# Kernel tuning notes

Hardware: AMD Instinct MI355X
Metric: run time of the kernel (lower is better)

The kernel has to match this reference:

```python
import jax, jax.numpy as jnp
import numpy as np

B, S, E = 2, 2048, 2048
H, HD = 32, 64          # n_heads, head_dim
KV, REP = 8, 4          # n_kv_head, n_kv_head_rep (H == KV*REP)
NEG = -1e9


def setup_inputs() -> dict:
    key = jax.random.key(0)
    ks = jax.random.split(key, 6)
    x = jax.random.normal(ks[0], (B, S, E), dtype=jnp.float32)
    # Llama RoPE tables: angles[p, i] = p / 10000^(2i/HD)
    inv_freq = 1.0 / (10000.0 ** (jnp.arange(0, HD, 2, dtype=jnp.float32) / HD))
    angles = jnp.arange(S, dtype=jnp.float32)[:, None] * inv_freq[None, :]  # [S, HD/2]
    cos, sin = jnp.cos(angles), jnp.sin(angles)
    # causal additive mask [S, S]
    mask = jnp.where(jnp.tril(jnp.ones((S, S), dtype=bool)), 0.0, NEG).astype(jnp.float32)
    sc = 0.02
    wq = jax.random.normal(ks[1], (E, H * HD), dtype=jnp.float32) * sc
    wk = jax.random.normal(ks[2], (E, KV * HD), dtype=jnp.float32) * sc
    wv = jax.random.normal(ks[3], (E, KV * HD), dtype=jnp.float32) * sc
    wo = jax.random.normal(ks[4], (H * HD, E), dtype=jnp.float32) * sc
    return {"x": x, "cos": cos, "sin": sin, "mask": mask,
            "wq": wq, "wk": wk, "wv": wv, "wo": wo, "start_pos": 0}


def _rope(t, cos, sin):
    # t: [B, S, h, HD]; rotate consecutive pairs (Llama complex convention)
    tp = t.reshape(t.shape[:-1] + (HD // 2, 2))
    t1, t2 = tp[..., 0], tp[..., 1]
    c = cos[None, :, None, :]
    s = sin[None, :, None, :]
    out = jnp.stack([t1 * c - t2 * s, t1 * s + t2 * c], axis=-1)
    return out.reshape(t.shape)


def reference(x, cos, sin, mask, wq, wk, wv, wo, start_pos):
    b, s, _ = x.shape
    q = (x @ wq).reshape(b, s, H, HD)
    k = (x @ wk).reshape(b, s, KV, HD)
    v = (x @ wv).reshape(b, s, KV, HD)
    q = _rope(q, cos, sin)
    k = _rope(k, cos, sin)
    # KV-cache: with start_pos=0 and full-seq prefill, the cache slice
    # [:, :start_pos+s] is exactly the freshly written k/v, so use them directly.
    # Grouped attention without materializing repeated K/V:
    # q -> [b, KV, REP, s, HD]; k,v -> [b, KV, s, HD]
    qg = q.transpose(0, 2, 1, 3).reshape(b, KV, REP, s, HD)
    kg = k.transpose(0, 2, 1, 3)
    vg = v.transpose(0, 2, 1, 3)
    scale = 1.0 / jnp.sqrt(jnp.float32(HD))
    scores = jnp.einsum('bgrqd,bgkd->bgrqk', qg, kg) * scale + mask
    attn = jax.nn.softmax(scores, axis=-1)
    og = jnp.einsum('bgrqk,bgkd->bgrqd', attn, vg)     # [b, KV, REP, s, HD]
    out = og.reshape(b, H, s, HD).transpose(0, 2, 1, 3).reshape(b, s, H * HD)
    return out @ wo
```

## Files before the change

### kernel.cpp

```cpp
#include <hip/hip_runtime.h>
#include <stdint.h>

#define S_LEN 2048
#define NTOK  4096
#define EMB   2048
#define NHEAD 32
#define HDIM  64
#define NKVH  8

typedef __bf16 bf16x8 __attribute__((ext_vector_type(8)));
typedef float  f32x4  __attribute__((ext_vector_type(4)));

#define AS1 __attribute__((address_space(1)))
#define AS3 __attribute__((address_space(3)))

#if __has_builtin(__builtin_amdgcn_exp2f)
#define EXP2(x) __builtin_amdgcn_exp2f(x)
#else
#define EXP2(x) exp2f(x)
#endif

#define QSCALE 0.1803368867f

__device__ __forceinline__ uint16_t f2bf(float f) {
  uint32_t u = __float_as_uint(f);
  u += 0x7fffu + ((u >> 16) & 1u);
  return (uint16_t)(u >> 16);
}
__device__ __forceinline__ float bf2f(uint16_t h) {
  return __uint_as_float(((uint32_t)h) << 16);
}
__device__ __forceinline__ void gld16(const void* g, void* l) {
  __builtin_amdgcn_global_load_lds((const AS1 uint32_t*)g, (AS3 uint32_t*)l, 16, 0, 0);
}
__device__ __forceinline__ f32x4 mfma16(bf16x8 a, bf16x8 b, f32x4 c) {
  return __builtin_amdgcn_mfma_f32_16x16x32_bf16(a, b, c, 0, 0, 0);
}

__global__ void k_cvt(const float* __restrict__ in, uint16_t* __restrict__ out) {
  int i = (blockIdx.x * 256 + threadIdx.x) * 4;
  float4 v = *(const float4*)(in + i);
  ushort4 o;
  o.x = f2bf(v.x); o.y = f2bf(v.y); o.z = f2bf(v.z); o.w = f2bf(v.w);
  *(ushort4*)(out + i) = o;
}

__global__ void k_transpose(const float* __restrict__ in, uint16_t* __restrict__ out,
                            int R, int C) {
  __shared__ float tile[32][33];
  int c0 = blockIdx.x * 32, r0 = blockIdx.y * 32;
  int tx = threadIdx.x & 31, ty = threadIdx.x >> 5;
#pragma unroll
  for (int j = 0; j < 32; j += 8)
    tile[ty + j][tx] = in[(size_t)(r0 + ty + j) * C + c0 + tx];
  __syncthreads();
#pragma unroll
  for (int j = 0; j < 32; j += 8)
    out[(size_t)(c0 + ty + j) * R + r0 + tx] = f2bf(tile[tx][ty + j]);
}

__global__ void k_transpose_v(const uint16_t* __restrict__ in, uint16_t* __restrict__ out) {
  __shared__ uint16_t tile[32][33];
  int s0 = blockIdx.x * 32, hd0 = blockIdx.y * 32, bh = blockIdx.z;
  int b = bh >> 3, kvh = bh & 7;
  int tx = threadIdx.x & 31, ty = threadIdx.x >> 5;
#pragma unroll
  for (int j = 0; j < 32; j += 8)
    tile[ty + j][tx] = in[((size_t)b * S_LEN + s0 + ty + j) * 512 + kvh * 64 + hd0 + tx];
  __syncthreads();
#pragma unroll
  for (int j = 0; j < 32; j += 8)
    out[((size_t)bh * 64 + hd0 + ty + j) * S_LEN + s0 + tx] = tile[tx][ty + j];
}

template <int N_REP, typename OUT_T>
__global__ __launch_bounds__(512, 2) void k_gemm256(
    const uint16_t* __restrict__ A, const uint16_t* __restrict__ BT,
    OUT_T* __restrict__ C, int M, int N, int K) {
  constexpr int ROUNDS = 4 + N_REP;
  __shared__ uint16_t lds[2][16384 + N_REP * 4096];
  const int tid = threadIdx.x, lane = tid & 63, w = tid >> 6;
  const int wm = w >> 2, wn = w & 3;
  const int l16 = lane & 15, lg = lane >> 4;
  const int nbn = N / (N_REP * 64);
  const int nwg = gridDim.x, cpx = nwg >> 3;
  const int swz = ((int)blockIdx.x & 7) * cpx + ((int)blockIdx.x >> 3);
  const int bm = (swz / nbn) * 256, bn = (swz % nbn) * (N_REP * 64);

  f32x4 acc[8][N_REP] = {};

  const int srow = tid >> 3, sslot = tid & 7;
  const int schunk = (sslot ^ (srow & 7)) * 8;
  const uint16_t* Ag = A + (size_t)(bm + srow) * K + schunk;
  const uint16_t* Bg = BT + (size_t)(bn + srow) * K + schunk;

  auto stage = [&](int d, int r, int k0) {
    if (r < 4) gld16(Ag + (size_t)r * 64 * K + k0, &lds[d][r * 4096 + tid * 8]);
    else       gld16(Bg + (size_t)(r - 4) * 64 * K + k0, &lds[d][16384 + (r - 4) * 4096 + tid * 8]);
  };
  auto lda = [&](int d, int mf, int s) -> bf16x8 {
    int row = wm * 128 + mf * 16 + l16;
    int slot = (s * 4 + lg) ^ (row & 7);
    return *(const bf16x8*)(&lds[d][row * 64 + slot * 8]);
  };
  auto ldb = [&](int d, int nf, int s) -> bf16x8 {
    int row = wn * (N_REP * 16) + nf * 16 + l16;
    int slot = (s * 4 + lg) ^ (row & 7);
    return *(const bf16x8*)(&lds[d][16384 + row * 64 + slot * 8]);
  };

  const int NT = K >> 6;
#pragma unroll
  for (int r = 0; r < ROUNDS; ++r) stage(0, r, 0);
#pragma unroll
  for (int r = 0; r < 4; ++r) if (1 < NT) stage(1, r, 64);
  asm volatile("s_waitcnt vmcnt(4)" ::: "memory");
  __builtin_amdgcn_s_barrier();

  for (int kt = 0; kt < NT; ++kt) {
    const int cur = kt & 1;
    const int nk0 = (kt + 1) << 6, nnk0 = (kt + 2) << 6;
    const bool m1 = (kt + 1 < NT), m2 = (kt + 2 < NT);
    bf16x8 a[4][2], b0[N_REP / 2][2], b1[N_REP / 2][2];
#pragma unroll
    for (int mi = 0; mi < 4; ++mi) { a[mi][0] = lda(cur, mi, 0); a[mi][1] = lda(cur, mi, 1); }
#pragma unroll
    for (int ni = 0; ni < N_REP / 2; ++ni) { b0[ni][0] = ldb(cur, ni, 0); b0[ni][1] = ldb(cur, ni, 1); }
    __builtin_amdgcn_s_barrier();
    asm volatile("s_waitcnt lgkmcnt(0)" ::: "memory");
    __builtin_amdgcn_sched_barrier(0);
    __builtin_amdgcn_s_setprio(1);
#pragma unroll
    for (int mi = 0; mi < 4; ++mi)
#pragma unroll
      for (int ni = 0; ni < N_REP / 2; ++ni) {
        acc[mi][ni] = mfma16(a[mi][0], b0[ni][0], acc[mi][ni]);
        acc[mi][ni] = mfma16(a[mi][1], b0[ni][1], acc[mi][ni]);
      }
    __builtin_amdgcn_s_setprio(0);
    __builtin_amdgcn_s_barrier();
#pragma unroll
    for (int ni = 0; ni < N_REP / 2; ++ni) { b1[ni][0] = ldb(cur, N_REP / 2 + ni, 0); b1[ni][1] = ldb(cur, N_REP / 2 + ni, 1); }
    if (m1) {
#pragma unroll
      for (int r = 4; r < 4 + N_REP / 2; ++r) stage(cur ^ 1, r, nk0);
    }
    __builtin_amdgcn_s_barrier();
    asm volatile("s_waitcnt lgkmcnt(0)" ::: "memory");
    __builtin_amdgcn_sched_barrier(0);
    __builtin_amdgcn_s_setprio(1);
#pragma unroll
    for (int mi = 0; mi < 4; ++mi)
#pragma unroll
      for (int ni = 0; ni < N_REP / 2; ++ni) {
        acc[mi][N_REP / 2 + ni] = mfma16(a[mi][0], b1[ni][0], acc[mi][N_REP / 2 + ni]);
        acc[mi][N_REP / 2 + ni] = mfma16(a[mi][1], b1[ni][1], acc[mi][N_REP / 2 + ni]);
      }
    __builtin_amdgcn_s_setprio(0);
    __builtin_amdgcn_s_barrier();
#pragma unroll
    for (int mi = 0; mi < 4; ++mi) { a[mi][0] = lda(cur, 4 + mi, 0); a[mi][1] = lda(cur, 4 + mi, 1); }
    if (m1) {
#pragma unroll
      for (int r = 4 + N_REP / 2; r < ROUNDS; ++r) stage(cur ^ 1, r, nk0);
    }
    __builtin_amdgcn_s_barrier();
    asm volatile("s_waitcnt lgkmcnt(0)" ::: "memory");
    __builtin_amdgcn_sched_barrier(0);
    __builtin_amdgcn_s_setprio(1);
#pragma unroll
    for (int mi = 0; mi < 4; ++mi)
#pragma unroll
      for (int ni = 0; ni < N_REP / 2; ++ni) {
        acc[4 + mi][N_REP / 2 + ni] = mfma16(a[mi][0], b1[ni][0], acc[4 + mi][N_REP / 2 + ni]);
        acc[4 + mi][N_REP / 2 + ni] = mfma16(a[mi][1], b1[ni][1], acc[4 + mi][N_REP / 2 + ni]);
      }
    __builtin_amdgcn_s_setprio(0);
    __builtin_amdgcn_s_barrier();
    if (m2) {
#pragma unroll
      for (int r = 0; r < 4; ++r) stage(cur, r, nnk0);
    }
    __builtin_amdgcn_s_setprio(1);
#pragma unroll
    for (int mi = 0; mi < 4; ++mi)
#pragma unroll
      for (int ni = 0; ni < N_REP / 2; ++ni) {
        acc[4 + mi][ni] = mfma16(a[mi][0], b0[ni][0], acc[4 + mi][ni]);
        acc[4 + mi][ni] = mfma16(a[mi][1], b0[ni][1], acc[4 + mi][ni]);
      }
    __builtin_amdgcn_s_setprio(0);
    if (m2) { asm volatile("s_waitcnt vmcnt(4)" ::: "memory"); }
    else    { asm volatile("s_waitcnt vmcnt(0)" ::: "memory"); }
    __builtin_amdgcn_s_barrier();
  }
#pragma unroll
  for (int mf = 0; mf < 8; ++mf)
#pragma unroll
    for (int nf = 0; nf < N_REP; ++nf)
#pragma unroll
      for (int r = 0; r < 4; ++r) {
        int row = bm + wm * 128 + mf * 16 + lg * 4 + r;
        int col = bn + wn * (N_REP * 16) + nf * 16 + l16;
        float v = acc[mf][nf][r];
        if constexpr (sizeof(OUT_T) == 4) C[(size_t)row * N + col] = v;
        else                              C[(size_t)row * N + col] = f2bf(v);
      }
}

__global__ void k_rope(const uint16_t* __restrict__ qkv, const float* __restrict__ cosT,
                       const float* __restrict__ sinT, uint16_t* __restrict__ qb,
                       uint16_t* __restrict__ kb, uint16_t* __restrict__ vb) {
  int idx = blockIdx.x * 256 + threadIdx.x;
  int row = idx / 1536;
  int col = (idx - row * 1536) * 2;
  int s = row & (S_LEN - 1);
  uint32_t vv = *(const uint32_t*)(qkv + (size_t)row * 3072 + col);
  float t1 = bf2f((uint16_t)vv), t2 = bf2f((uint16_t)(vv >> 16));
  if (col < 2048) {
    int i = (col & 63) >> 1;
    float c = cosT[s * 32 + i] * QSCALE, sn = sinT[s * 32 + i] * QSCALE;
    uint32_t o = (uint32_t)f2bf(t1 * c - t2 * sn) | ((uint32_t)f2bf(t1 * sn + t2 * c) << 16);
    *(uint32_t*)(qb + (size_t)row * 2048 + col) = o;
  } else if (col < 2560) {
    int cc = col - 2048;
    int i = (cc & 63) >> 1;
    float c = cosT[s * 32 + i], sn = sinT[s * 32 + i];
    uint32_t o = (uint32_t)f2bf(t1 * c - t2 * sn) | ((uint32_t)f2bf(t1 * sn + t2 * c) << 16);
    *(uint32_t*)(kb + (size_t)row * 512 + cc) = o;
  } else {
    int cc = col - 2560;
    *(uint32_t*)(vb + (size_t)row * 512 + cc) = vv;
  }
}

template <bool MASKED>
__device__ __forceinline__ void tile_compute(
    const uint16_t* Kc, const uint16_t* Vc, const bf16x8 qf[2][2], bf16x8 onesv,
    int l16, int lg, int kv0, int qb0,
    float m_r[2], f32x4 lacc[2], f32x4 acc[2][4]) {
  f32x4 st[2][4] = {};
  __builtin_amdgcn_s_setprio(1);
#pragma unroll
  for (int c = 0; c < 4; ++c) {
    int row = c * 16 + l16, sw = row & 7;
    bf16x8 ka  = *(const bf16x8*)(Kc + row * 64 + ((lg ^ sw) * 8));
    bf16x8 kb2 = *(const bf16x8*)(Kc + row * 64 + (((4 | lg) ^ sw) * 8));
#pragma unroll
    for (int qc = 0; qc < 2; ++qc) {
      st[qc][c] = mfma16(ka,  qf[qc][0], st[qc][c]);
      st[qc][c] = mfma16(kb2, qf[qc][1], st[qc][c]);
    }
  }
  __builtin_amdgcn_s_setprio(0);
  bf16x8 pu[2][2];
#pragma unroll
  for (int qc = 0; qc < 2; ++qc) {
    const int qrow = qb0 + qc * 16 + l16;
    float sv[4][4];
#pragma unroll
    for (int c = 0; c < 4; ++c)
#pragma unroll
      for (int r = 0; r < 4; ++r) {
        float s = st[qc][c][r];
        if (MASKED && (kv0 + c * 16 + lg * 4 + r > qrow)) s = -1e30f;
        sv[c][r] = s;
      }
    float m0 = fmaxf(fmaxf(sv[0][0], sv[0][1]), fmaxf(sv[0][2], sv[0][3]));
    float m1 = fmaxf(fmaxf(sv[1][0], sv[1][1]), fmaxf(sv[1][2], sv[1][3]));
    float m2 = fmaxf(fmaxf(sv[2][0], sv[2][1]), fmaxf(sv[2][2], sv[2][3]));
    float m3 = fmaxf(fmaxf(sv[3][0], sv[3][1]), fmaxf(sv[3][2], sv[3][3]));
    float mx = fmaxf(fmaxf(m0, m1), fmaxf(m2, m3));
    mx = fmaxf(mx, __shfl_xor(mx, 16));
    mx = fmaxf(mx, __shfl_xor(mx, 32));
    if (!__all(mx - m_r[qc] <= 8.0f)) {
      float m_new = fmaxf(m_r[qc], mx);
      float alpha = EXP2(m_r[qc] - m_new);
      float al[4];
#pragma unroll
      for (int r = 0; r < 4; ++r) al[r] = __shfl(alpha, lg * 4 + r);
#pragma unroll
      for (int n = 0; n < 4; ++n)
#pragma unroll
        for (int r = 0; r < 4; ++r) acc[qc][n][r] *= al[r];
#pragma unroll
      for (int r = 0; r < 4; ++r) lacc[qc][r] *= al[r];
      m_r[qc] = m_new;
    }
    float pf[4][4];
#pragma unroll
    for (int c = 0; c < 4; ++c)
#pragma unroll
      for (int r = 0; r < 4; ++r)
        pf[c][r] = EXP2(sv[c][r] - m_r[qc]);
#pragma unroll
    for (int cc = 0; cc < 2; ++cc)
#pragma unroll
      for (int e = 0; e < 8; ++e)
        ((__bf16*)&pu[qc][cc])[e] = (__bf16)pf[cc * 2 + (e >> 2)][e & 3];
  }
  __builtin_amdgcn_s_setprio(1);
#pragma unroll
  for (int cc = 0; cc < 2; ++cc) {
    lacc[0] = mfma16(pu[0][cc], onesv, lacc[0]);
    lacc[1] = mfma16(pu[1][cc], onesv, lacc[1]);
#pragma unroll
    for (int n = 0; n < 4; ++n) {
      int row = n * 16 + l16, sw2 = row & 7;
      int k0 = cc * 32 + lg * 4, k1 = k0 + 16;
      const char* base = (const char*)Vc + row * 128;
      union { uint64_t q[2]; bf16x8 v; } vu;
      vu.q[0] = *(const uint64_t*)(base + (((k0 >> 3) ^ sw2) << 4) + ((k0 & 7) << 1));
      vu.q[1] = *(const uint64_t*)(base + (((k1 >> 3) ^ sw2) << 4) + ((k1 & 7) << 1));
      acc[0][n] = mfma16(pu[0][cc], vu.v, acc[0][n]);
      acc[1][n] = mfma16(pu[1][cc], vu.v, acc[1][n]);
    }
  }
  __builtin_amdgcn_s_setprio(0);
}

__global__ __launch_bounds__(512, 4) void k_flash(
    const uint16_t* __restrict__ Qb, const uint16_t* __restrict__ Kb,
    const uint16_t* __restrict__ VT, uint16_t* __restrict__ Ob) {
  __shared__ uint16_t Ks[3][4096];
  __shared__ uint16_t Vs[3][4096];
  const int lidx = blockIdx.x;
  const int qt = (lidx < 256) ? 31 - (lidx & 31) : (lidx & 31);
  const int gb = lidx >> 5;
  const int g = gb & 7, b = gb >> 3;
  const int tid = threadIdx.x, lane = tid & 63, w = tid >> 6;
  const int l16 = lane & 15, lg = lane >> 4;
  const int h = g * 4 + (w >> 1);
  const int qb0 = qt * 64 + (w & 1) * 32;
  bf16x8 qf[2][2];
#pragma unroll
  for (int qc = 0; qc < 2; ++qc) {
    const size_t tokq = (size_t)b * S_LEN + qb0 + qc * 16 + l16;
    qf[qc][0] = *(const bf16x8*)(Qb + tokq * 2048 + h * 64 + lg * 8);
    qf[qc][1] = *(const bf16x8*)(Qb + tokq * 2048 + h * 64 + 32 + lg * 8);
  }
  bf16x8 onesv;
#pragma unroll
  for (int e = 0; e < 8; ++e) ((__bf16*)&onesv)[e] = (__bf16)1.0f;

  const int srow = tid >> 3, shc = tid & 7;
  const int swz = (shc ^ (srow & 7)) * 8;
  const uint16_t* Kg = Kb + ((size_t)b * S_LEN + srow) * 512 + g * 64 + swz;
  const uint16_t* Vg = VT + ((size_t)(b * 8 + g) * 64 + srow) * S_LEN + swz;

  float m_r[2] = {-1e30f, -1e30f};
  f32x4 lacc[2] = {};
  f32x4 acc[2][4] = {};
  const int nt = qt + 1;

  auto stage = [&](int t, int buf) {
    const size_t kv0 = (size_t)t * 64;
    gld16(Kg + kv0 * 512, &Ks[buf][tid * 8]);
    gld16(Vg + kv0, &Vs[buf][tid * 8]);
  };

  stage(0, 0);
  stage(nt > 1 ? 1 : 0, 1);

  int cur = 0;
  for (int t = 0; t < nt; ++t) {
    asm volatile("s_waitcnt vmcnt(2)" ::: "memory");
    __builtin_amdgcn_s_barrier();
    {
      int ts = t + 2 < nt ? t + 2 : nt - 1;
      int bufn = cur + 2; if (bufn >= 3) bufn -= 3;
      stage(ts, bufn);
    }
    if (t == qt)
      tile_compute<true >(Ks[cur], Vs[cur], qf, onesv, l16, lg, t * 64, qb0, m_r, lacc, acc);
    else
      tile_compute<false>(Ks[cur], Vs[cur], qf, onesv, l16, lg, t * 64, qb0, m_r, lacc, acc);
    cur = cur + 1 < 3 ? cur + 1 : 0;
  }
#pragma unroll
  for (int qc = 0; qc < 2; ++qc) {
    float li[4];
#pragma unroll
    for (int r = 0; r < 4; ++r) li[r] = 1.0f / lacc[qc][r];
#pragma unroll
    for (int n = 0; n < 4; ++n)
#pragma unroll
      for (int r = 0; r < 4; ++r) {
        int qo = qb0 + qc * 16 + lg * 4 + r;
        Ob[((size_t)b * S_LEN + qo) * 2048 + h * 64 + n * 16 + l16] =
            f2bf(acc[qc][n][r] * li[r]);
      }
  }
}

extern "C" void kernel_launch(void* const* d_in, const int* in_sizes, int n_in,
                              void* d_out, int out_size, void* d_ws, size_t ws_size,
                              hipStream_t stream) {
  const float* x    = (const float*)d_in[0];
  const float* cosT = (const float*)d_in[1];
  const float* sinT = (const float*)d_in[2];
  const float* wq   = (const float*)d_in[4];
  const float* wk   = (const float*)d_in[5];
  const float* wv   = (const float*)d_in[6];
  const float* wo   = (const float*)d_in[7];
  float* out = (float*)d_out;

  char* ws = (char*)d_ws;
  size_t off = 0;
  auto alloc = [&](size_t bytes) {
    void* p = ws + off;
    off += (bytes + 255) & ~(size_t)255;
    return p;
  };
  uint16_t* xb   = (uint16_t*)alloc((size_t)NTOK * EMB * 2);
  uint16_t* wT   = (uint16_t*)alloc((size_t)3072 * 2048 * 2);
  uint16_t* woT  = (uint16_t*)alloc((size_t)2048 * 2048 * 2);
  uint16_t* qkvb = (uint16_t*)alloc((size_t)NTOK * 3072 * 2);
  uint16_t* qb   = (uint16_t*)alloc((size_t)NTOK * 2048 * 2);
  uint16_t* kb   = (uint16_t*)alloc((size_t)NTOK * 512 * 2);
  uint16_t* vb   = (uint16_t*)alloc((size_t)NTOK * 512 * 2);
  uint16_t* ob   = xb;
  uint16_t* vT   = qkvb;

  k_cvt<<<(NTOK * EMB) / 1024, 256, 0, stream>>>(x, xb);
  k_transpose<<<dim3(64, 64), 256, 0, stream>>>(wq, wT, 2048, 2048);
  k_transpose<<<dim3(16, 64), 256, 0, stream>>>(wk, wT + (size_t)2048 * 2048, 2048, 512);
  k_transpose<<<dim3(16, 64), 256, 0, stream>>>(wv, wT + (size_t)2560 * 2048, 2048, 512);
  k_transpose<<<dim3(64, 64), 256, 0, stream>>>(wo, woT, 2048, 2048);

  k_gemm256<4, uint16_t><<<192, 512, 0, stream>>>(xb, wT, qkvb, 4096, 3072, 2048);
  k_rope<<<(NTOK * 1536) / 256, 256, 0, stream>>>(qkvb, cosT, sinT, qb, kb, vb);
  k_transpose_v<<<dim3(64, 2, 16), 256, 0, stream>>>(vb, vT);
  k_flash<<<dim3(512), 512, 0, stream>>>(qb, kb, vT, ob);
  k_gemm256<2, float><<<256, 512, 0, stream>>>(ob, woT, out, 4096, 2048, 2048);
}
```

Before: 204.5 us.

## Split flash attention into smaller 256-thread blocks with 16 query rows per wave

The attention kernel is reworked so each wave handles a single 16-row query chunk instead of two, and each block covers two heads of a 32-row query tile with 256 threads. This gives 2048 blocks instead of 512. Blocks are ordered longest causal range first, and each thread now stages two 16-byte chunks each for K and V, with the wait count adjusted to match. The aim is finer-grained work for better load balance and occupancy across the causal triangle. In exchange, each staged K/V tile is shared by fewer heads and query rows, so K/V traffic and LDS reads per unit of MFMA work go up.

```diff
diff --git a/kernel.cpp b/kernel.cpp
--- a/kernel.cpp
+++ b/kernel.cpp
@@ -235,75 +235,67 @@
 }
 
 template <bool MASKED>
-__device__ __forceinline__ void tile_compute(
-    const uint16_t* Kc, const uint16_t* Vc, const bf16x8 qf[2][2], bf16x8 onesv,
-    int l16, int lg, int kv0, int qb0,
-    float m_r[2], f32x4 lacc[2], f32x4 acc[2][4]) {
-  f32x4 st[2][4] = {};
+__device__ __forceinline__ void tile_compute16(
+    const uint16_t* Kc, const uint16_t* Vc, const bf16x8 qf[2], bf16x8 onesv,
+    int l16, int lg, int kv0, int qrow,
+    float& m_r, f32x4& lacc, f32x4 acc[4]) {
+  f32x4 st[4] = {};
   __builtin_amdgcn_s_setprio(1);
 #pragma unroll
   for (int c = 0; c < 4; ++c) {
     int row = c * 16 + l16, sw = row & 7;
     bf16x8 ka  = *(const bf16x8*)(Kc + row * 64 + ((lg ^ sw) * 8));
     bf16x8 kb2 = *(const bf16x8*)(Kc + row * 64 + (((4 | lg) ^ sw) * 8));
-#pragma unroll
-    for (int qc = 0; qc < 2; ++qc) {
-      st[qc][c] = mfma16(ka,  qf[qc][0], st[qc][c]);
-      st[qc][c] = mfma16(kb2, qf[qc][1], st[qc][c]);
-    }
+    st[c] = mfma16(ka,  qf[0], st[c]);
+    st[c] = mfma16(kb2, qf[1], st[c]);
   }
   __builtin_amdgcn_s_setprio(0);
-  bf16x8 pu[2][2];
-#pragma unroll
-  for (int qc = 0; qc < 2; ++qc) {
-    const int qrow = qb0 + qc * 16 + l16;
-    float sv[4][4];
-#pragma unroll
-    for (int c = 0; c < 4; ++c)
-#pragma unroll
-      for (int r = 0; r < 4; ++r) {
-        float s = st[qc][c][r];
-        if (MASKED && (kv0 + c * 16 + lg * 4 + r > qrow)) s = -1e30f;
-        sv[c][r] = s;
-      }
-    float m0 = fmaxf(fmaxf(sv[0][0], sv[0][1]), fmaxf(sv[0][2], sv[0][3]));
-    float m1 = fmaxf(fmaxf(sv[1][0], sv[1][1]), fmaxf(sv[1][2], sv[1][3]));
-    float m2 = fmaxf(fmaxf(sv[2][0], sv[2][1]), fmaxf(sv[2][2], sv[2][3]));
-    float m3 = fmaxf(fmaxf(sv[3][0], sv[3][1]), fmaxf(sv[3][2], sv[3][3]));
-    float mx = fmaxf(fmaxf(m0, m1), fmaxf(m2, m3));
-    mx = fmaxf(mx, __shfl_xor(mx, 16));
-    mx = fmaxf(mx, __shfl_xor(mx, 32));
-    if (!__all(mx - m_r[qc] <= 8.0f)) {
-      float m_new = fmaxf(m_r[qc], mx);
-      float alpha = EXP2(m_r[qc] - m_new);
-      float al[4];
-#pragma unroll
-      for (int r = 0; r < 4; ++r) al[r] = __shfl(alpha, lg * 4 + r);
-#pragma unroll
-      for (int n = 0; n < 4; ++n)
-#pragma unroll
-        for (int r = 0; r < 4; ++r) acc[qc][n][r] *= al[r];
-#pragma unroll
-      for (int r = 0; r < 4; ++r) lacc[qc][r] *= al[r];
-      m_r[qc] = m_new;
-    }
-    float pf[4][4];
-#pragma unroll
-    for (int c = 0; c < 4; ++c)
-#pragma unroll
-      for (int r = 0; r < 4; ++r)
-        pf[c][r] = EXP2(sv[c][r] - m_r[qc]);
-#pragma unroll
-    for (int cc = 0; cc < 2; ++cc)
-#pragma unroll
-      for (int e = 0; e < 8; ++e)
-        ((__bf16*)&pu[qc][cc])[e] = (__bf16)pf[cc * 2 + (e >> 2)][e & 3];
-  }
+  float sv[4][4];
+#pragma unroll
+  for (int c = 0; c < 4; ++c)
+#pragma unroll
+    for (int r = 0; r < 4; ++r) {
+      float s = st[c][r];
+      if (MASKED && (kv0 + c * 16 + lg * 4 + r > qrow)) s = -1e30f;
+      sv[c][r] = s;
+    }
+  float m0 = fmaxf(fmaxf(sv[0][0], sv[0][1]), fmaxf(sv[0][2], sv[0][3]));
+  float m1 = fmaxf(fmaxf(sv[1][0], sv[1][1]), fmaxf(sv[1][2], sv[1][3]));
+  float m2 = fmaxf(fmaxf(sv[2][0], sv[2][1]), fmaxf(sv[2][2], sv[2][3]));
+  float m3 = fmaxf(fmaxf(sv[3][0], sv[3][1]), fmaxf(sv[3][2], sv[3][3]));
+  float mx = fmaxf(fmaxf(m0, m1), fmaxf(m2, m3));
+  mx = fmaxf(mx, __shfl_xor(mx, 16));
+  mx = fmaxf(mx, __shfl_xor(mx, 32));
+  if (!__all(mx - m_r <= 8.0f)) {
+    float m_new = fmaxf(m_r, mx);
+    float alpha = EXP2(m_r - m_new);
+    float al[4];
+#pragma unroll
+    for (int r = 0; r < 4; ++r) al[r] = __shfl(alpha, lg * 4 + r);
+#pragma unroll
+    for (int n = 0; n < 4; ++n)
+#pragma unroll
+      for (int r = 0; r < 4; ++r) acc[n][r] *= al[r];
+#pragma unroll
+    for (int r = 0; r < 4; ++r) lacc[r] *= al[r];
+    m_r = m_new;
+  }
+  float pf[4][4];
+#pragma unroll
+  for (int c = 0; c < 4; ++c)
+#pragma unroll
+    for (int r = 0; r < 4; ++r)
+      pf[c][r] = EXP2(sv[c][r] - m_r);
+  bf16x8 pu[2];
+#pragma unroll
+  for (int cc = 0; cc < 2; ++cc)
+#pragma unroll
+    for (int e = 0; e < 8; ++e)
+      ((__bf16*)&pu[cc])[e] = (__bf16)pf[cc * 2 + (e >> 2)][e & 3];
   __builtin_amdgcn_s_setprio(1);
 #pragma unroll
   for (int cc = 0; cc < 2; ++cc) {
-    lacc[0] = mfma16(pu[0][cc], onesv, lacc[0]);
-    lacc[1] = mfma16(pu[1][cc], onesv, lacc[1]);
+    lacc = mfma16(pu[cc], onesv, lacc);
 #pragma unroll
     for (int n = 0; n < 4; ++n) {
       int row = n * 16 + l16, sw2 = row & 7;
@@ -312,33 +304,32 @@
       union { uint64_t q[2]; bf16x8 v; } vu;
       vu.q[0] = *(const uint64_t*)(base + (((k0 >> 3) ^ sw2) << 4) + ((k0 & 7) << 1));
       vu.q[1] = *(const uint64_t*)(base + (((k1 >> 3) ^ sw2) << 4) + ((k1 & 7) << 1));
-      acc[0][n] = mfma16(pu[0][cc], vu.v, acc[0][n]);
-      acc[1][n] = mfma16(pu[1][cc], vu.v, acc[1][n]);
+      acc[n] = mfma16(pu[cc], vu.v, acc[n]);
     }
   }
   __builtin_amdgcn_s_setprio(0);
 }
 
-__global__ __launch_bounds__(512, 4) void k_flash(
+__global__ __launch_bounds__(256, 3) void k_flash(
     const uint16_t* __restrict__ Qb, const uint16_t* __restrict__ Kb,
     const uint16_t* __restrict__ VT, uint16_t* __restrict__ Ob) {
   __shared__ uint16_t Ks[3][4096];
   __shared__ uint16_t Vs[3][4096];
-  const int lidx = blockIdx.x;
-  const int qt = (lidx < 256) ? 31 - (lidx & 31) : (lidx & 31);
-  const int gb = lidx >> 5;
+  const int j = 63 - ((int)blockIdx.x >> 5);
+  const int low5 = blockIdx.x & 31;
+  const int gb = low5 >> 1, hh = low5 & 1;
   const int g = gb & 7, b = gb >> 3;
   const int tid = threadIdx.x, lane = tid & 63, w = tid >> 6;
   const int l16 = lane & 15, lg = lane >> 4;
-  const int h = g * 4 + (w >> 1);
-  const int qb0 = qt * 64 + (w & 1) * 32;
-  bf16x8 qf[2][2];
-#pragma unroll
-  for (int qc = 0; qc < 2; ++qc) {
-    const size_t tokq = (size_t)b * S_LEN + qb0 + qc * 16 + l16;
-    qf[qc][0] = *(const bf16x8*)(Qb + tokq * 2048 + h * 64 + lg * 8);
-    qf[qc][1] = *(const bf16x8*)(Qb + tokq * 2048 + h * 64 + 32 + lg * 8);
-  }
+  const int h = g * 4 + hh * 2 + (w >> 1);
+  const int qb0 = j * 32 + (w & 1) * 16;
+  const int qrow = qb0 + l16;
+  const size_t tokq = (size_t)b * S_LEN + qrow;
+
+  bf16x8 qf[2];
+  qf[0] = *(const bf16x8*)(Qb + tokq * 2048 + h * 64 + lg * 8);
+  qf[1] = *(const bf16x8*)(Qb + tokq * 2048 + h * 64 + 32 + lg * 8);
+
   bf16x8 onesv;
 #pragma unroll
   for (int e = 0; e < 8; ++e) ((__bf16*)&onesv)[e] = (__bf16)1.0f;
@@ -348,15 +339,19 @@
   const uint16_t* Kg = Kb + ((size_t)b * S_LEN + srow) * 512 + g * 64 + swz;
   const uint16_t* Vg = VT + ((size_t)(b * 8 + g) * 64 + srow) * S_LEN + swz;
 
-  float m_r[2] = {-1e30f, -1e30f};
-  f32x4 lacc[2] = {};
-  f32x4 acc[2][4] = {};
-  const int nt = qt + 1;
+  float m_r = -1e30f;
+  f32x4 lacc = {};
+  f32x4 acc[4] = {};
+  const int nt = (j >> 1) + 1;
 
   auto stage = [&](int t, int buf) {
     const size_t kv0 = (size_t)t * 64;
-    gld16(Kg + kv0 * 512, &Ks[buf][tid * 8]);
-    gld16(Vg + kv0, &Vs[buf][tid * 8]);
+    uint16_t* kd = &Ks[buf][tid * 8];
+    uint16_t* vd = &Vs[buf][tid * 8];
+    gld16(Kg + kv0 * 512, kd);
+    gld16(Kg + (kv0 + 32) * 512, kd + 2048);
+    gld16(Vg + kv0, vd);
+    gld16(Vg + kv0 + (size_t)32 * S_LEN, vd + 2048);
   };
 
   stage(0, 0);
@@ -364,33 +359,30 @@
 
   int cur = 0;
   for (int t = 0; t < nt; ++t) {
-    asm volatile("s_waitcnt vmcnt(2)" ::: "memory");
+    asm volatile("s_waitcnt vmcnt(4)" ::: "memory");
     __builtin_amdgcn_s_barrier();
     {
       int ts = t + 2 < nt ? t + 2 : nt - 1;
       int bufn = cur + 2; if (bufn >= 3) bufn -= 3;
       stage(ts, bufn);
     }
-    if (t == qt)
-      tile_compute<true >(Ks[cur], Vs[cur], qf, onesv, l16, lg, t * 64, qb0, m_r, lacc, acc);
+    if (t == nt - 1)
+      tile_compute16<true >(Ks[cur], Vs[cur], qf, onesv, l16, lg, t * 64, qrow, m_r, lacc, acc);
     else
-      tile_compute<false>(Ks[cur], Vs[cur], qf, onesv, l16, lg, t * 64, qb0, m_r, lacc, acc);
+      tile_compute16<false>(Ks[cur], Vs[cur], qf, onesv, l16, lg, t * 64, qrow, m_r, lacc, acc);
     cur = cur + 1 < 3 ? cur + 1 : 0;
   }
-#pragma unroll
-  for (int qc = 0; qc < 2; ++qc) {
-    float li[4];
-#pragma unroll
-    for (int r = 0; r < 4; ++r) li[r] = 1.0f / lacc[qc][r];
-#pragma unroll
-    for (int n = 0; n < 4; ++n)
-#pragma unroll
-      for (int r = 0; r < 4; ++r) {
-        int qo = qb0 + qc * 16 + lg * 4 + r;
-        Ob[((size_t)b * S_LEN + qo) * 2048 + h * 64 + n * 16 + l16] =
-            f2bf(acc[qc][n][r] * li[r]);
-      }
-  }
+  float li[4];
+#pragma unroll
+  for (int r = 0; r < 4; ++r) li[r] = 1.0f / lacc[r];
+#pragma unroll
+  for (int n = 0; n < 4; ++n)
+#pragma unroll
+    for (int r = 0; r < 4; ++r) {
+      int qo = qb0 + lg * 4 + r;
+      Ob[((size_t)b * S_LEN + qo) * 2048 + h * 64 + n * 16 + l16] =
+          f2bf(acc[n][r] * li[r]);
+    }
 }
 
 extern "C" void kernel_launch(void* const* d_in, const int* in_sizes, int n_in,
@@ -431,6 +423,6 @@
   k_gemm256<4, uint16_t><<<192, 512, 0, stream>>>(xb, wT, qkvb, 4096, 3072, 2048);
   k_rope<<<(NTOK * 1536) / 256, 256, 0, stream>>>(qkvb, cosT, sinT, qb, kb, vb);
   k_transpose_v<<<dim3(64, 2, 16), 256, 0, stream>>>(vb, vT);
-  k_flash<<<dim3(512), 512, 0, stream>>>(qb, kb, vT, ob);
+  k_flash<<<dim3(2048), 256, 0, stream>>>(qb, kb, vT, ob);
   k_gemm256<2, float><<<256, 512, 0, stream>>>(ob, woT, out, 4096, 2048, 2048);
 }
```

After: 210.4 us. +2.9%, slower.
